# Optimization experiments

Hardware: AMD Instinct MI355X
Metric: run time of the kernel (lower is better)

The kernel has to match this reference:

```python
import jax, jax.numpy as jnp
import numpy as np

D_MODEL = 1024
N_HEADS = 16
D_K = D_MODEL // N_HEADS
THETA = 10000.0
B, S = 4, 2048


def _rope(x, positions):
    # x: [B, H, S, D_K]; positions: [S] int
    half = D_K // 2
    inv_freq = THETA ** (-jnp.arange(0, half, dtype=jnp.float32) * 2.0 / D_K)  # [half]
    ang = positions.astype(jnp.float32)[:, None] * inv_freq[None, :]  # [S, half]
    cos = jnp.cos(ang)[None, None, :, :]
    sin = jnp.sin(ang)[None, None, :, :]
    x_even = x[..., 0::2]
    x_odd = x[..., 1::2]
    out_even = x_even * cos - x_odd * sin
    out_odd = x_even * sin + x_odd * cos
    # interleave back to original layout
    out = jnp.stack([out_even, out_odd], axis=-1).reshape(x.shape)
    return out


def setup_inputs() -> dict:
    key = jax.random.key(0)
    ks = jax.random.split(key, 5)
    scale = 1.0 / np.sqrt(D_MODEL)
    return {
        "x": jax.random.normal(ks[0], (B, S, D_MODEL), dtype=jnp.float32),
        "token_positions": jnp.arange(S, dtype=jnp.int64 if jax.config.jax_enable_x64 else jnp.int32),
        "Wq": jax.random.normal(ks[1], (D_MODEL, D_MODEL), dtype=jnp.float32) * scale,
        "Wk": jax.random.normal(ks[2], (D_MODEL, D_MODEL), dtype=jnp.float32) * scale,
        "Wv": jax.random.normal(ks[3], (D_MODEL, D_MODEL), dtype=jnp.float32) * scale,
        "Wo": jax.random.normal(ks[4], (D_MODEL, D_MODEL), dtype=jnp.float32) * scale,
    }


def reference(x, token_positions, Wq, Wk, Wv, Wo):
    bsz, seq_len, _ = x.shape
    # projections (Linear_Transform: y = x @ W^T, no bias)
    def proj(W):
        h = jnp.einsum("bsd,ed->bse", x, W)
        return h.reshape(bsz, seq_len, N_HEADS, D_K).transpose(0, 2, 1, 3)  # [B,H,S,Dk]
    Q = proj(Wq)
    K = proj(Wk)
    V = proj(Wv)
    Q = _rope(Q, token_positions)
    K = _rope(K, token_positions)
    # scaled dot product attention with causal mask
    scores = jnp.einsum("bhqd,bhkd->bhqk", Q, K) / jnp.sqrt(jnp.float32(D_K))
    causal = jnp.tril(jnp.ones((seq_len, seq_len), dtype=bool))  # [S,S]
    scores = jnp.where(causal[None, None, :, :], scores, -jnp.inf)
    attn = jax.nn.softmax(scores, axis=-1)
    out = jnp.einsum("bhqk,bhkd->bhqd", attn, V)
    out = out.transpose(0, 2, 1, 3).reshape(bsz, seq_len, D_MODEL)
    return jnp.einsum("bsd,ed->bse", out, Wo)
```

## Files before the change

kernel.cpp:

```cpp
#include <hip/hip_runtime.h>
#include <hip/hip_bf16.h>
#include <cstdint>
#include <cstddef>

typedef __attribute__((ext_vector_type(4))) float f32x4;
typedef __attribute__((ext_vector_type(8))) short bf16x8;
typedef unsigned int u32;
typedef unsigned short u16;


__device__ __forceinline__ u16 f2bf(float x) {
  u32 u = __builtin_bit_cast(u32, x);
  u += 0x7fffu + ((u >> 16) & 1u);
  return (u16)(u >> 16);
}

__device__ __forceinline__ u32 cvt_pk_bf16(float lo, float hi) {
  u32 r;
  asm("v_cvt_pk_bf16_f32 %0, %1, %2" : "=v"(r) : "v"(lo), "v"(hi));
  return r;
}

__device__ __forceinline__ void gl_lds16(const void* g, void* l) {
  __builtin_amdgcn_global_load_lds(
      (const __attribute__((address_space(1))) u32*)(uintptr_t)g,
      (__attribute__((address_space(3))) u32*)(u32)(uintptr_t)l,
      16, 0, 0);
}

#define MFMA16(a, b, c) __builtin_amdgcn_mfma_f32_16x16x32_bf16((a), (b), (c), 0, 0, 0)


__global__ void cast_f32_bf16_v4(const float* __restrict__ src, u16* __restrict__ dst, int n4) {
  int i = blockIdx.x * 256 + threadIdx.x;
  if (i >= n4) return;
  const float4 v = reinterpret_cast<const float4*>(src)[i];
  union { u16 s[4]; uint2 u; } o;
  o.s[0] = f2bf(v.x); o.s[1] = f2bf(v.y); o.s[2] = f2bf(v.z); o.s[3] = f2bf(v.w);
  reinterpret_cast<uint2*>(dst)[i] = o.u;
}


__global__ void rope_table_k(const int* __restrict__ pos, float2* __restrict__ cs) {
  int idx = blockIdx.x * 256 + threadIdx.x;
  int s = idx >> 5, i = idx & 31;
  float inv = powf(10000.0f, -(float)i * (1.0f / 32.0f));
  float ang = (float)pos[s] * inv;
  cs[idx] = float2{cosf(ang), sinf(ang)};
}


__global__ __launch_bounds__(256, 2)
void gemm_qkv(const u16* __restrict__ A, const u16* __restrict__ B,
              const float2* __restrict__ cs, u16* __restrict__ Qr,
              u16* __restrict__ Kr, u16* __restrict__ Vt, float qscale) {
  const int K = 1024;
  __shared__ u16 a_lds[2][128 * 32];
  __shared__ u16 b_lds[2][128 * 32];
  const int tid = threadIdx.x;
  const int l = tid & 63;
  const int w = tid >> 6;
  const int wm = w >> 1, wn = w & 1;
  const int bm = blockIdx.y, bn = blockIdx.x;

  const u16* Ab = A + (size_t)bm * 128 * K;
  const u16* Bb = B + (size_t)bn * 128 * K;

  auto stage = [&](int bq, int k0) {
#pragma unroll
    for (int half = 0; half < 2; ++half) {
      int t = half * 256 + tid;
      int row = t >> 2, slot = t & 3;
      int sp = slot ^ ((row >> 1) & 3);
      gl_lds16(Ab + (size_t)row * K + k0 + sp * 8, &a_lds[bq][t * 8]);
      gl_lds16(Bb + (size_t)row * K + k0 + sp * 8, &b_lds[bq][t * 8]);
    }
  };

  const f32x4 fz = {0.f, 0.f, 0.f, 0.f};
  f32x4 acc[4][4];
#pragma unroll
  for (int mi = 0; mi < 4; ++mi)
#pragma unroll
    for (int ni = 0; ni < 4; ++ni) acc[mi][ni] = fz;

  const int nk = K >> 5;
  stage(0, 0);
  int buf = 0;
  for (int kt = 0; kt < nk; ++kt) {
    __syncthreads();
    if (kt + 1 < nk) stage(buf ^ 1, (kt + 1) * 32);
    bf16x8 af[4], bf[4];
#pragma unroll
    for (int mi = 0; mi < 4; ++mi) {
      int row = wm * 64 + mi * 16 + (l & 15);
      int sp = (l >> 4) ^ ((row >> 1) & 3);
      af[mi] = *(const bf16x8*)&a_lds[buf][row * 32 + sp * 8];
    }
#pragma unroll
    for (int ni = 0; ni < 4; ++ni) {
      int row = wn * 64 + ni * 16 + (l & 15);
      int sp = (l >> 4) ^ ((row >> 1) & 3);
      bf[ni] = *(const bf16x8*)&b_lds[buf][row * 32 + sp * 8];
    }
#pragma unroll
    for (int mi = 0; mi < 4; ++mi)
#pragma unroll
      for (int ni = 0; ni < 4; ++ni)
        acc[mi][ni] = MFMA16(af[mi], bf[ni], acc[mi][ni]);
    buf ^= 1;
  }

  const int sector = bn >> 3;
  const int colb = ((bn & 7) << 7) + wn * 64;
  const int c = l & 15, h4 = l >> 4;

  if (sector == 2) {
#pragma unroll
    for (int mi = 0; mi < 4; ++mi) {
      int row = bm * 128 + wm * 64 + mi * 16 + 4 * h4;
      int b_ = row >> 11, s = row & 2047;
#pragma unroll
      for (int ni = 0; ni < 4; ++ni) {
        int cv = colb + ni * 16 + c;
        int hh = cv >> 6, dk = cv & 63;
        f32x4 v = acc[mi][ni];
        uint2 st;
        st.x = cvt_pk_bf16(v[0], v[1]);
        st.y = cvt_pk_bf16(v[2], v[3]);
        *(uint2*)&Vt[(((size_t)b_ * 16 + hh) << 17) + ((size_t)dk << 11) + s] = st;
      }
    }
  } else {
    u16* dst = sector ? Kr : Qr;
    const float scale = sector ? 1.0f : qscale;
#pragma unroll
    for (int mi = 0; mi < 4; ++mi) {
      int row0 = bm * 128 + wm * 64 + mi * 16 + 4 * h4;
#pragma unroll
      for (int ni = 0; ni < 4; ++ni) {
        int cv = colb + ni * 16 + c;
        int hh = cv >> 6, i2 = cv & 63;
        f32x4 v = acc[mi][ni];
        f32x4 pv;
#pragma unroll
        for (int j = 0; j < 4; ++j) pv[j] = __shfl_xor(v[j], 1);
        if (!(l & 1)) {
#pragma unroll
          for (int j = 0; j < 4; ++j) {
            int r = row0 + j, s = r & 2047, b_ = r >> 11;
            float2 t = cs[(s << 5) + (i2 >> 1)];
            float oe = (v[j] * t.x - pv[j] * t.y) * scale;
            float oo = (v[j] * t.y + pv[j] * t.x) * scale;
            *(u32*)&dst[(((size_t)(b_ * 16 + hh) * 2048 + s) << 6) + i2] =
                cvt_pk_bf16(oe, oo);
          }
        }
      }
    }
  }
}


__global__ __launch_bounds__(256, 2)
void gemm_bt(const u16* __restrict__ A, const u16* __restrict__ B,
             float* __restrict__ C, int M, int N, int K) {
  __shared__ u16 a_lds[2][128 * 32];
  __shared__ u16 b_lds[2][128 * 32];
  const int tid = threadIdx.x;
  const int l = tid & 63;
  const int w = tid >> 6;
  const int wm = w >> 1, wn = w & 1;
  const int bm = blockIdx.y, bn = blockIdx.x;

  const u16* Ab = A + (size_t)bm * 128 * K;
  const u16* Bb = B + (size_t)bn * 128 * K;

  auto stage = [&](int bq, int k0) {
#pragma unroll
    for (int half = 0; half < 2; ++half) {
      int t = half * 256 + tid;
      int row = t >> 2, slot = t & 3;
      int sp = slot ^ ((row >> 1) & 3);
      gl_lds16(Ab + (size_t)row * K + k0 + sp * 8, &a_lds[bq][t * 8]);
      gl_lds16(Bb + (size_t)row * K + k0 + sp * 8, &b_lds[bq][t * 8]);
    }
  };

  const f32x4 fz = {0.f, 0.f, 0.f, 0.f};
  f32x4 acc[4][4];
#pragma unroll
  for (int mi = 0; mi < 4; ++mi)
#pragma unroll
    for (int ni = 0; ni < 4; ++ni) acc[mi][ni] = fz;

  const int nk = K >> 5;
  stage(0, 0);
  int buf = 0;
  for (int kt = 0; kt < nk; ++kt) {
    __syncthreads();
    if (kt + 1 < nk) stage(buf ^ 1, (kt + 1) * 32);
    bf16x8 af[4], bf[4];
#pragma unroll
    for (int mi = 0; mi < 4; ++mi) {
      int row = wm * 64 + mi * 16 + (l & 15);
      int sp = (l >> 4) ^ ((row >> 1) & 3);
      af[mi] = *(const bf16x8*)&a_lds[buf][row * 32 + sp * 8];
    }
#pragma unroll
    for (int ni = 0; ni < 4; ++ni) {
      int row = wn * 64 + ni * 16 + (l & 15);
      int sp = (l >> 4) ^ ((row >> 1) & 3);
      bf[ni] = *(const bf16x8*)&b_lds[buf][row * 32 + sp * 8];
    }
#pragma unroll
    for (int mi = 0; mi < 4; ++mi)
#pragma unroll
      for (int ni = 0; ni < 4; ++ni)
        acc[mi][ni] = MFMA16(af[mi], bf[ni], acc[mi][ni]);
    buf ^= 1;
  }

#pragma unroll
  for (int mi = 0; mi < 4; ++mi) {
    int rbase = bm * 128 + wm * 64 + mi * 16 + ((l >> 4) << 2);
#pragma unroll
    for (int ni = 0; ni < 4; ++ni) {
      int col = bn * 128 + wn * 64 + ni * 16 + (l & 15);
      f32x4 v = acc[mi][ni];
#pragma unroll
      for (int j = 0; j < 4; ++j)
        C[(size_t)(rbase + j) * N + col] = v[j];
    }
  }
}


__global__ __launch_bounds__(256, 4)
void attn_k(const u16* __restrict__ Q, const u16* __restrict__ K,
            const u16* __restrict__ V, u16* __restrict__ O) {
  const int S = 2048;
  __shared__ u16 q_lds[64 * 64];
  __shared__ u16 k_lds[2][64 * 64];
  __shared__ u16 v_lds[2][64 * 64];

  const int tid = threadIdx.x, l = tid & 63, w = tid >> 6;
  const int c = l & 15, h = l >> 4;

  const int wg = blockIdx.x;
  const int idx = (wg & 7) * 128 + (wg >> 3);
  const int bh = idx >> 4, pairI = idx & 15;

  const u16* Kb = K + (size_t)bh * S * 64;
  const u16* Vb = V + (size_t)bh * 64 * S;
  const int b = bh >> 4, hd = bh & 15;
  const f32x4 fz = {0.f, 0.f, 0.f, 0.f};

  int bperm[4];
#pragma unroll
  for (int tt = 0; tt < 4; ++tt)
    bperm[tt] = ((((l & 16) << 1) | ((tt >> 1) << 4) | c) << 2);

#pragma unroll 1
  for (int ph = 0; ph < 2; ++ph) {
    const int qi = ph ? (31 - pairI) : pairI;
    const int q0 = qi * 64;
    const int nkv = qi + 1;
    const u16* Qb = Q + ((size_t)bh * S + q0) * 64;

#pragma unroll
    for (int half = 0; half < 2; ++half) {
      int t = half * 256 + tid;
      int row = t >> 3, slot = t & 7;
      int sp = slot ^ (row & 7);
      gl_lds16(Qb + row * 64 + sp * 8, &q_lds[t * 8]);
      gl_lds16(Kb + (size_t)row * 64 + sp * 8, &k_lds[0][t * 8]);
      gl_lds16(Vb + (size_t)row * S + sp * 8, &v_lds[0][t * 8]);
    }
    __syncthreads();

    bf16x8 qf[2];
#pragma unroll
    for (int ks = 0; ks < 2; ++ks) {
      int row = w * 16 + c;
      int sp = (4 * ks + h) ^ (row & 7);
      qf[ks] = *(const bf16x8*)&q_lds[row * 64 + sp * 8];
    }

    f32x4 oacc[4];
#pragma unroll
    for (int ni = 0; ni < 4; ++ni) oacc[ni] = fz;
    float m_run = -1e30f, l_run = 0.f;

    int buf = 0;
    for (int t = 0; t < nkv; ++t) {
      if (t + 1 < nkv) {
        int kv0 = (t + 1) * 64;
#pragma unroll
        for (int half = 0; half < 2; ++half) {
          int tt = half * 256 + tid;
          int row = tt >> 3, slot = tt & 7;
          int sp = slot ^ (row & 7);
          gl_lds16(Kb + (size_t)(kv0 + row) * 64 + sp * 8, &k_lds[buf ^ 1][tt * 8]);
          gl_lds16(Vb + (size_t)row * S + kv0 + sp * 8, &v_lds[buf ^ 1][tt * 8]);
        }
      }

      f32x4 sc[4];
#pragma unroll
      for (int kvb = 0; kvb < 4; ++kvb) sc[kvb] = fz;
#pragma unroll
      for (int ks = 0; ks < 2; ++ks)
#pragma unroll
        for (int kvb = 0; kvb < 4; ++kvb) {
          int row = kvb * 16 + c;
          int sp = (4 * ks + h) ^ (row & 7);
          bf16x8 kf = *(const bf16x8*)&k_lds[buf][row * 64 + sp * 8];
          sc[kvb] = MFMA16(kf, qf[ks], sc[kvb]);
        }

      if (t == qi) {
        int qg = q0 + w * 16 + c;
#pragma unroll
        for (int kvb = 0; kvb < 4; ++kvb)
#pragma unroll
          for (int j = 0; j < 4; ++j) {
            int kvg = t * 64 + kvb * 16 + 4 * h + j;
            if (kvg > qg) sc[kvb][j] = -1e30f;
          }
      }

      float mx = -1e30f;
#pragma unroll
      for (int kvb = 0; kvb < 4; ++kvb)
#pragma unroll
        for (int j = 0; j < 4; ++j) mx = fmaxf(mx, sc[kvb][j]);
      mx = fmaxf(mx, __shfl_xor(mx, 16));
      mx = fmaxf(mx, __shfl_xor(mx, 32));

      const bool norescale = __all(mx <= m_run);
      float mnew = norescale ? m_run : fmaxf(m_run, mx);
      float ps = 0.f;
#pragma unroll
      for (int kvb = 0; kvb < 4; ++kvb)
#pragma unroll
        for (int j = 0; j < 4; ++j) {
          float e = exp2f(sc[kvb][j] - mnew);
          sc[kvb][j] = e;
          ps += e;
        }
      ps += __shfl_xor(ps, 16);
      ps += __shfl_xor(ps, 32);

      if (norescale) {
        l_run += ps;
      } else {
        float alpha = exp2f(m_run - mnew);
        l_run = l_run * alpha + ps;
        m_run = mnew;
        float aj[4];
#pragma unroll
        for (int j = 0; j < 4; ++j) aj[j] = __shfl(alpha, 20 * h + j);
#pragma unroll
        for (int ni = 0; ni < 4; ++ni)
#pragma unroll
          for (int j = 0; j < 4; ++j) oacc[ni][j] *= aj[j];
      }

      u32 pk[4][2];
#pragma unroll
      for (int kvb = 0; kvb < 4; ++kvb) {
        pk[kvb][0] = cvt_pk_bf16(sc[kvb][0], sc[kvb][1]);
        pk[kvb][1] = cvt_pk_bf16(sc[kvb][2], sc[kvb][3]);
      }

#pragma unroll
      for (int ks = 0; ks < 2; ++ks) {
        union { u32 u[4]; bf16x8 v; } af;
#pragma unroll
        for (int tt = 0; tt < 4; ++tt) {
          u32 lo = (u32)__builtin_amdgcn_ds_bpermute(bperm[tt], (int)pk[2 * ks][tt & 1]);
          u32 hi = (u32)__builtin_amdgcn_ds_bpermute(bperm[tt], (int)pk[2 * ks + 1][tt & 1]);
          af.u[tt] = (l & 32) ? hi : lo;
        }
#pragma unroll
        for (int ni = 0; ni < 4; ++ni) {
          int row = ni * 16 + c;
          int sp = (4 * ks + h) ^ (row & 7);
          bf16x8 vf = *(const bf16x8*)&v_lds[buf][row * 64 + sp * 8];
          oacc[ni] = MFMA16(af.v, vf, oacc[ni]);
        }
      }

      __syncthreads();
      buf ^= 1;
    }

    float invl[4];
#pragma unroll
    for (int j = 0; j < 4; ++j)
      invl[j] = 1.f / __shfl(l_run, 20 * h + j);
#pragma unroll
    for (int ni = 0; ni < 4; ++ni)
#pragma unroll
      for (int j = 0; j < 4; ++j) {
        int srow = q0 + w * 16 + 4 * h + j;
        int dk = ni * 16 + c;
        O[((size_t)(b * 2048 + srow) << 10) + hd * 64 + dk] = f2bf(oacc[ni][j] * invl[j]);
      }
    __syncthreads();
  }
}


extern "C" void kernel_launch(void* const* d_in, const int* in_sizes, int n_in,
                              void* d_out, int out_size, void* d_ws, size_t ws_size,
                              hipStream_t stream) {
  (void)in_sizes; (void)n_in; (void)out_size; (void)ws_size;
  const float* x  = (const float*)d_in[0];
  const int* pos  = (const int*)d_in[1];
  const float* Wq = (const float*)d_in[2];
  const float* Wk = (const float*)d_in[3];
  const float* Wv = (const float*)d_in[4];
  const float* Wo = (const float*)d_in[5];
  float* out = (float*)d_out;

  const int S = 2048, D = 1024;
  const size_t M = (size_t)4 * S;

  char* ws = (char*)d_ws;
  size_t off = 0;
  auto alloc = [&](size_t bytes) {
    void* p = ws + off;
    off += (bytes + 255) & ~(size_t)255;
    return p;
  };
  u16* xb   = (u16*)alloc(M * D * 2);
  u16* wqb  = (u16*)alloc((size_t)D * D * 2);
  u16* wkb  = (u16*)alloc((size_t)D * D * 2);
  u16* wvb  = (u16*)alloc((size_t)D * D * 2);
  u16* wob  = (u16*)alloc((size_t)D * D * 2);
  u16* Qr   = (u16*)alloc(M * D * 2);
  u16* Kr   = (u16*)alloc(M * D * 2);
  u16* Vt   = (u16*)alloc(M * D * 2);
  u16* Ob   = (u16*)alloc(M * D * 2);
  float2* csT = (float2*)alloc((size_t)S * 32 * 8);

  const int nx4 = (int)(M * D / 4);
  const int nw4 = D * D / 4;
  cast_f32_bf16_v4<<<(nx4 + 255) / 256, 256, 0, stream>>>(x, xb, nx4);
  cast_f32_bf16_v4<<<(nw4 + 255) / 256, 256, 0, stream>>>(Wq, wqb, nw4);
  cast_f32_bf16_v4<<<(nw4 + 255) / 256, 256, 0, stream>>>(Wk, wkb, nw4);
  cast_f32_bf16_v4<<<(nw4 + 255) / 256, 256, 0, stream>>>(Wv, wvb, nw4);
  cast_f32_bf16_v4<<<(nw4 + 255) / 256, 256, 0, stream>>>(Wo, wob, nw4);
  rope_table_k<<<(S * 32) / 256, 256, 0, stream>>>(pos, csT);

  const float QSCALE = 0.125f * 1.4426950408889634f;

  gemm_qkv<<<dim3(24, (unsigned)(M / 128)), 256, 0, stream>>>(
      xb, wqb, csT, Qr, Kr, Vt, QSCALE);
  attn_k<<<1024, 256, 0, stream>>>(Qr, Kr, Vt, Ob);
  gemm_bt<<<dim3(8, (unsigned)(M / 128)), 256, 0, stream>>>(Ob, wob, out, (int)M, D, D);
}
```

Baseline: 214.1 us.

## Fuse cast kernels and restructure attention KV pipeline with explicit waits and priorities

The five f32-to-bf16 cast launches are merged into one kernel that uses packed bf16 conversion. The attention kernel loads Q fragments straight from global memory instead of going through LDS. KV staging is now synchronised with explicit vmcnt waits and raw s_barriers, MFMA sections are wrapped in s_setprio to raise wave priority, and the trailing per-phase syncthreads is removed. These changes target launch overhead, LDS footprint and barrier stalls, at the cost of relying on exact vmcnt counting being correct.

```diff
diff --git a/kernel.cpp b/kernel.cpp
--- a/kernel.cpp
+++ b/kernel.cpp
@@ -31,13 +31,24 @@
 #define MFMA16(a, b, c) __builtin_amdgcn_mfma_f32_16x16x32_bf16((a), (b), (c), 0, 0, 0)
 
 
-__global__ void cast_f32_bf16_v4(const float* __restrict__ src, u16* __restrict__ dst, int n4) {
-  int i = blockIdx.x * 256 + threadIdx.x;
-  if (i >= n4) return;
-  const float4 v = reinterpret_cast<const float4*>(src)[i];
-  union { u16 s[4]; uint2 u; } o;
-  o.s[0] = f2bf(v.x); o.s[1] = f2bf(v.y); o.s[2] = f2bf(v.z); o.s[3] = f2bf(v.w);
-  reinterpret_cast<uint2*>(dst)[i] = o.u;
+__global__ void cast_all_k(const float* __restrict__ x, const float* __restrict__ wq,
+                           const float* __restrict__ wk, const float* __restrict__ wv,
+                           const float* __restrict__ wo, u16* __restrict__ xb,
+                           u16* __restrict__ wqb, u16* __restrict__ wkb,
+                           u16* __restrict__ wvb, u16* __restrict__ wob) {
+  int blk = blockIdx.x;
+  const float* s; u16* d; int i;
+  if (blk < 8192)       { s = x;  d = xb;  i = blk * 256; }
+  else if (blk < 9216)  { s = wq; d = wqb; i = (blk - 8192) * 256; }
+  else if (blk < 10240) { s = wk; d = wkb; i = (blk - 9216) * 256; }
+  else if (blk < 11264) { s = wv; d = wvb; i = (blk - 10240) * 256; }
+  else                  { s = wo; d = wob; i = (blk - 11264) * 256; }
+  i += threadIdx.x;
+  const float4 v = reinterpret_cast<const float4*>(s)[i];
+  uint2 o;
+  o.x = cvt_pk_bf16(v.x, v.y);
+  o.y = cvt_pk_bf16(v.z, v.w);
+  reinterpret_cast<uint2*>(d)[i] = o;
 }
 
 
@@ -240,7 +251,6 @@
 void attn_k(const u16* __restrict__ Q, const u16* __restrict__ K,
             const u16* __restrict__ V, u16* __restrict__ O) {
   const int S = 2048;
-  __shared__ u16 q_lds[64 * 64];
   __shared__ u16 k_lds[2][64 * 64];
   __shared__ u16 v_lds[2][64 * 64];
 
@@ -260,6 +270,17 @@
 #pragma unroll
   for (int tt = 0; tt < 4; ++tt)
     bperm[tt] = ((((l & 16) << 1) | ((tt >> 1) << 4) | c) << 2);
+
+  auto stageKV = [&](int bq, int kv0) {
+#pragma unroll
+    for (int half = 0; half < 2; ++half) {
+      int t = half * 256 + tid;
+      int row = t >> 3, slot = t & 7;
+      int sp = slot ^ (row & 7);
+      gl_lds16(Kb + (size_t)(kv0 + row) * 64 + sp * 8, &k_lds[bq][t * 8]);
+      gl_lds16(Vb + (size_t)row * S + kv0 + sp * 8, &v_lds[bq][t * 8]);
+    }
+  };
 
 #pragma unroll 1
   for (int ph = 0; ph < 2; ++ph) {
@@ -268,24 +289,12 @@
     const int nkv = qi + 1;
     const u16* Qb = Q + ((size_t)bh * S + q0) * 64;
 
-#pragma unroll
-    for (int half = 0; half < 2; ++half) {
-      int t = half * 256 + tid;
-      int row = t >> 3, slot = t & 7;
-      int sp = slot ^ (row & 7);
-      gl_lds16(Qb + row * 64 + sp * 8, &q_lds[t * 8]);
-      gl_lds16(Kb + (size_t)row * 64 + sp * 8, &k_lds[0][t * 8]);
-      gl_lds16(Vb + (size_t)row * S + sp * 8, &v_lds[0][t * 8]);
-    }
-    __syncthreads();
-
     bf16x8 qf[2];
 #pragma unroll
-    for (int ks = 0; ks < 2; ++ks) {
-      int row = w * 16 + c;
-      int sp = (4 * ks + h) ^ (row & 7);
-      qf[ks] = *(const bf16x8*)&q_lds[row * 64 + sp * 8];
-    }
+    for (int ks = 0; ks < 2; ++ks)
+      qf[ks] = *(const bf16x8*)(Qb + (size_t)(w * 16 + c) * 64 + ks * 32 + h * 8);
+    __builtin_amdgcn_sched_barrier(0);
+    stageKV(0, 0);
 
     f32x4 oacc[4];
 #pragma unroll
@@ -293,22 +302,23 @@
     float m_run = -1e30f, l_run = 0.f;
 
     int buf = 0;
+#pragma unroll 1
     for (int t = 0; t < nkv; ++t) {
       if (t + 1 < nkv) {
-        int kv0 = (t + 1) * 64;
-#pragma unroll
-        for (int half = 0; half < 2; ++half) {
-          int tt = half * 256 + tid;
-          int row = tt >> 3, slot = tt & 7;
-          int sp = slot ^ (row & 7);
-          gl_lds16(Kb + (size_t)(kv0 + row) * 64 + sp * 8, &k_lds[buf ^ 1][tt * 8]);
-          gl_lds16(Vb + (size_t)row * S + kv0 + sp * 8, &v_lds[buf ^ 1][tt * 8]);
-        }
-      }
+        stageKV(buf ^ 1, (t + 1) * 64);
+        __builtin_amdgcn_sched_barrier(0);
+        asm volatile("s_waitcnt vmcnt(4)" ::: "memory");
+      } else {
+        asm volatile("s_waitcnt vmcnt(0)" ::: "memory");
+      }
+      __builtin_amdgcn_sched_barrier(0);
+      __builtin_amdgcn_s_barrier();
+      __builtin_amdgcn_sched_barrier(0);
 
       f32x4 sc[4];
 #pragma unroll
       for (int kvb = 0; kvb < 4; ++kvb) sc[kvb] = fz;
+      __builtin_amdgcn_s_setprio(1);
 #pragma unroll
       for (int ks = 0; ks < 2; ++ks)
 #pragma unroll
@@ -318,6 +328,7 @@
           bf16x8 kf = *(const bf16x8*)&k_lds[buf][row * 64 + sp * 8];
           sc[kvb] = MFMA16(kf, qf[ks], sc[kvb]);
         }
+      __builtin_amdgcn_s_setprio(0);
 
       if (t == qi) {
         int qg = q0 + w * 16 + c;
@@ -383,6 +394,7 @@
           u32 hi = (u32)__builtin_amdgcn_ds_bpermute(bperm[tt], (int)pk[2 * ks + 1][tt & 1]);
           af.u[tt] = (l & 32) ? hi : lo;
         }
+        __builtin_amdgcn_s_setprio(1);
 #pragma unroll
         for (int ni = 0; ni < 4; ++ni) {
           int row = ni * 16 + c;
@@ -390,9 +402,12 @@
           bf16x8 vf = *(const bf16x8*)&v_lds[buf][row * 64 + sp * 8];
           oacc[ni] = MFMA16(af.v, vf, oacc[ni]);
         }
-      }
-
-      __syncthreads();
+        __builtin_amdgcn_s_setprio(0);
+      }
+
+      __builtin_amdgcn_sched_barrier(0);
+      __builtin_amdgcn_s_barrier();
+      __builtin_amdgcn_sched_barrier(0);
       buf ^= 1;
     }
 
@@ -408,7 +423,6 @@
         int dk = ni * 16 + c;
         O[((size_t)(b * 2048 + srow) << 10) + hd * 64 + dk] = f2bf(oacc[ni][j] * invl[j]);
       }
-    __syncthreads();
   }
 }
 
@@ -446,13 +460,7 @@
   u16* Ob   = (u16*)alloc(M * D * 2);
   float2* csT = (float2*)alloc((size_t)S * 32 * 8);
 
-  const int nx4 = (int)(M * D / 4);
-  const int nw4 = D * D / 4;
-  cast_f32_bf16_v4<<<(nx4 + 255) / 256, 256, 0, stream>>>(x, xb, nx4);
-  cast_f32_bf16_v4<<<(nw4 + 255) / 256, 256, 0, stream>>>(Wq, wqb, nw4);
-  cast_f32_bf16_v4<<<(nw4 + 255) / 256, 256, 0, stream>>>(Wk, wkb, nw4);
-  cast_f32_bf16_v4<<<(nw4 + 255) / 256, 256, 0, stream>>>(Wv, wvb, nw4);
-  cast_f32_bf16_v4<<<(nw4 + 255) / 256, 256, 0, stream>>>(Wo, wob, nw4);
+  cast_all_k<<<12288, 256, 0, stream>>>(x, Wq, Wk, Wv, Wo, xb, wqb, wkb, wvb, wob);
   rope_table_k<<<(S * 32) / 256, 256, 0, stream>>>(pos, csT);
 
   const float QSCALE = 0.125f * 1.4426950408889634f;
```

After: 207.6 us. -3.0%, faster.
